# Kernel tuning notes

Hardware: AMD Instinct MI355X
Metric: run time of the kernel (lower is better)

Reference implementation:

```python
import jax, jax.numpy as jnp
import numpy as np

# ---- constants mirroring the torch module ----
OSAMP = 8            # temporal oversampling factor
MAX_ITER = 10        # forward solver iterations (LBFGS replaced by fixed GD)
NEG_SHIFT = 2 * OSAMP
OTP = 5              # baseline frames subtracted from ctc/aif
C_SHARP = 500.0      # sharpness constant C=500 in fermi_ir_func
LR = 0.1             # fixed step size for the deterministic forward solve


def interp_linear_1d(x, size):
    # interp_linear_1D: linear upsampling along last (time) axis
    return jax.image.resize(x, x.shape[:-1] + (size,), method='linear')


def fermi_ir(eta, t_os):
    # eta: [B,3,H,W] = (amplitude A, decay rate k, delay t0); t_os: [Tos]
    tsh = t_os - t_os[NEG_SHIFT]                    # negative time shift
    A = eta[:, 0][..., None]                        # [B,H,W,1]
    k = eta[:, 1][..., None]
    t0 = eta[:, 2][..., None]
    step = jax.nn.sigmoid(C_SHARP * tsh)            # sharp causal onset (C=500)
    return A * jax.nn.sigmoid(k * (t0 - tsh)) * step  # [B,H,W,Tos]


def convolve(aif, ir):
    # linear convolution along time via FFT; output aligned with neg_shift offset
    Tos = ir.shape[-1]
    n = 2 * Tos
    Fa = jnp.fft.rfft(aif, n=n, axis=-1)            # [B,1,1,n/2+1]
    Fi = jnp.fft.rfft(ir, n=n, axis=-1)             # [B,H,W,n/2+1]
    full = jnp.fft.irfft(Fa * Fi, n=n, axis=-1)
    return jax.lax.dynamic_slice_in_dim(full, NEG_SHIFT, Tos, axis=-1)


def make_objective(ctc, aif, time, eta_prior, lambda_reg):
    # preprocessing from FermiDataConsLBFGS.forward
    aif = aif - aif[..., :OTP].mean(-1, keepdims=True)
    ctc = ctc - ctc[..., :OTP].mean(-1, keepdims=True)
    Tos = OSAMP * ctc.shape[-1]
    aif_os = interp_linear_1d(aif, Tos)
    ctc_os = interp_linear_1d(ctc, Tos)
    t_os = interp_linear_1d(time, Tos)
    ctc_dc = ctc_os[..., ::OSAMP]                   # [B,H,W,T]
    C_nn = (eta_prior ** 2).sum(axis=(0, 2, 3), keepdims=True)  # [1,3,1,1]
    C_dc = (ctc_dc ** 2).sum()
    sp_lam = jax.nn.softplus(lambda_reg).squeeze()

    def F_obj(eta):  # FermiDConsObj.__call__ (OD disabled: indx_dc = all frames)
        ir = fermi_ir(eta, t_os)
        ctc_est = convolve(aif_os, ir)[..., ::OSAMP] / OSAMP
        dc = ((ctc_dc - ctc_est) ** 2 / C_dc).sum()
        reg = sp_lam * (((eta - eta_prior) ** 2) / C_nn).sum()
        pos = (jax.nn.relu(-eta) ** 2).sum()
        return dc + reg + pos
    return F_obj


def setup_inputs():
    key = jax.random.key(0)
    k1, k2, k3, k4 = jax.random.split(key, 4)
    B, H, W, T = 1, 128, 128, 64
    ctc = jax.random.normal(k1, (B, H, W, T), jnp.float32) * 0.1
    aif = jax.random.uniform(k2, (B, 1, 1, T), jnp.float32)
    time = jnp.arange(T, dtype=jnp.float32)
    seg = jnp.ones((B, H, W), jnp.int32)
    eta_nn = jax.random.uniform(k3, (B, 3, H, W), jnp.float32)
    lambda_reg = jax.random.normal(k4, (1,), jnp.float32)
    return {"ctc": ctc, "aif": aif, "time": time, "seg": seg,
            "eta_nn": eta_nn, "lambda_reg": lambda_reg}


def reference(ctc, aif, time, seg, eta_nn, lambda_reg):
    # seg only affects the (disabled) outlier-detection path
    F_obj = make_objective(ctc, aif, time, eta_nn, lambda_reg)
    gradF = jax.grad(F_obj)

    def step(eta, _):
        return eta - LR * gradF(eta), None

    eta_pi, _ = jax.lax.scan(step, eta_nn, None, length=MAX_ITER)
    return eta_pi
```

## Files before the change

### kernel.cpp

```cpp
#include <hip/hip_runtime.h>
#include <math.h>

#define T_IN 64
#define NPIX 16384
#define MAX_ITER 10
#define NSLOT 43

typedef _Float16 half8_t __attribute__((ext_vector_type(8)));
typedef __fp16   fp16x2  __attribute__((ext_vector_type(2)));
typedef float    f32x4   __attribute__((ext_vector_type(4)));
typedef int      i32x4   __attribute__((ext_vector_type(4)));

union H8 { half8_t v; fp16x2 h2[4]; i32x4 i4; };

__device__ __forceinline__ float rcp_fast(float x) { return __builtin_amdgcn_rcpf(x); }

__device__ __forceinline__ float exp2_fast(float x) {
#if __has_builtin(__builtin_amdgcn_exp2f)
    return __builtin_amdgcn_exp2f(x);
#else
    return exp2f(x);
#endif
}

__constant__ constexpr int NTMIN[16] = {0,0,0,0,0,1,1,1,1,2,2,2,2,3,3,3};
__constant__ constexpr int TOFS[16]  = {0,4,8,12,16,20,23,26,29,32,34,36,38,40,41,42};
__constant__ constexpr int POS[16]   = {0,0,4,4,8,8,12,11,15,14,18,16,20,18,22,19};
#define NBREG 23

template<int KT>
__device__ __forceinline__ void buildTile(float T0, float c, float cT0, float ch,
        float r, float r2, float r3, int q,
        const float (&d10s)[8], const float (&tse)[8],
        H8& F0h, H8& F1h, H8& F2h) {
    constexpr int J = KT >> 1;
    float  x[8];
    fp16x2 d1h[4];
    float  d10 = T0 - d10s[J];
    const fp16x2 c1 = {(__fp16)0.25f, (__fp16)0.25f};
    const fp16x2 c2 = {(__fp16)0.50f, (__fp16)0.50f};
    const fp16x2 c3 = {(__fp16)0.75f, (__fp16)0.75f};
    bool arith = true;
    if constexpr (KT == 0 || KT == 15) {
        bool flat = (KT == 0) ? (q == 0) : (q == 3);
        if (flat) {
            arith = false;
            #pragma unroll
            for (int j = 0; j < 8; ++j)
                x[j] = exp2_fast(fmaf(-c, tse[j], cT0));
            #pragma unroll
            for (int jj = 0; jj < 4; ++jj)
                d1h[jj] = __builtin_amdgcn_cvt_pkrtz(T0 - tse[2*jj],
                                                     T0 - tse[2*jj+1]);
        }
    }
    if (arith) {
        float a0 = fmaf(-c, d10s[J], cT0);
        x[0] = exp2_fast(a0);
        x[4] = exp2_fast(a0 - ch);
        x[1] = x[0]*r; x[2] = x[0]*r2; x[3] = x[0]*r3;
        x[5] = x[4]*r; x[6] = x[4]*r2; x[7] = x[4]*r3;
        fp16x2 D0 = __builtin_amdgcn_cvt_pkrtz(d10, d10 - 0.125f);
        d1h[0] = D0;
        d1h[1] = D0 - c1;
        d1h[2] = D0 - c2;
        d1h[3] = D0 - c3;
    }
    #pragma unroll
    for (int jj = 0; jj < 4; ++jj) {
        float s1a = rcp_fast(1.0f + x[2*jj]);
        float s1b = rcp_fast(1.0f + x[2*jj+1]);
        fp16x2 sh = __builtin_amdgcn_cvt_pkrtz(s1a, s1b);
        fp16x2 eh = sh - sh*sh;
        F0h.h2[jj] = sh;
        F1h.h2[jj] = eh * d1h[jj];
        F2h.h2[jj] = eh;
    }
}

template<int KT, int NT, int BI>
struct MfmaNT {
    static __device__ __forceinline__ void run(const i32x4 (&Breg)[NBREG],
            const H8 (&F0p)[4], const H8 (&F1p)[4], const H8 (&F2p)[4],
            f32x4 (&acc)[3][4]) {
        constexpr int idx = POS[KT] + NT - NTMIN[KT];
        H8 bh; bh.i4 = Breg[idx];
        if constexpr (KT < 2) {
            const f32x4 Z = (f32x4){0.f, 0.f, 0.f, 0.f};
            acc[0][NT] = __builtin_amdgcn_mfma_f32_16x16x32_f16(F0p[BI].v, bh.v, Z, 0, 0, 0);
            acc[1][NT] = __builtin_amdgcn_mfma_f32_16x16x32_f16(F1p[BI].v, bh.v, Z, 0, 0, 0);
            acc[2][NT] = __builtin_amdgcn_mfma_f32_16x16x32_f16(F2p[BI].v, bh.v, Z, 0, 0, 0);
        } else {
            acc[0][NT] = __builtin_amdgcn_mfma_f32_16x16x32_f16(F0p[BI].v, bh.v, acc[0][NT], 0, 0, 0);
            acc[1][NT] = __builtin_amdgcn_mfma_f32_16x16x32_f16(F1p[BI].v, bh.v, acc[1][NT], 0, 0, 0);
            acc[2][NT] = __builtin_amdgcn_mfma_f32_16x16x32_f16(F2p[BI].v, bh.v, acc[2][NT], 0, 0, 0);
        }
        if constexpr (NT + 1 < 4)
            MfmaNT<KT, NT+1, BI>::run(Breg, F0p, F1p, F2p, acc);
    }
};

template<int H, int S>
struct PipeB {
    static __device__ __forceinline__ void run(float T0, float c, float cT0, float ch,
            float r, float r2, float r3, int q,
            const float (&d10s)[8], const float (&tse)[8],
            const i32x4 (&Breg)[NBREG],
            H8 (&F0p)[4], H8 (&F1p)[4], H8 (&F2p)[4],
            f32x4 (&acc)[3][4]) {
        if constexpr (2*S+2 < 8)
            buildTile<H + 2*(2*S+2)>(T0, c, cT0, ch, r, r2, r3, q, d10s, tse,
                F0p[(2*S+2)&3], F1p[(2*S+2)&3], F2p[(2*S+2)&3]);
        if constexpr (2*S+3 < 8)
            buildTile<H + 2*(2*S+3)>(T0, c, cT0, ch, r, r2, r3, q, d10s, tse,
                F0p[(2*S+3)&3], F1p[(2*S+3)&3], F2p[(2*S+3)&3]);
        MfmaNT<H + 4*S,     NTMIN[H + 4*S],     (2*S)&3  >::run(Breg, F0p, F1p, F2p, acc);
        MfmaNT<H + 4*S + 2, NTMIN[H + 4*S + 2], (2*S+1)&3>::run(Breg, F0p, F1p, F2p, acc);
        if constexpr (S + 1 < 4)
            PipeB<H, S+1>::run(T0, c, cT0, ch, r, r2, r3, q, d10s, tse,
                               Breg, F0p, F1p, F2p, acc);
    }
};

template<int H>
__device__ __forceinline__ void pipeAcc(float T0, float c, float cT0, float ch,
        float r, float r2, float r3, int q,
        const float (&d10s)[8], const float (&tse)[8],
        const i32x4 (&Breg)[NBREG], f32x4 (&acc)[3][4]) {
    H8 F0p[4], F1p[4], F2p[4];
    buildTile<H>  (T0, c, cT0, ch, r, r2, r3, q, d10s, tse, F0p[0], F1p[0], F2p[0]);
    buildTile<H+2>(T0, c, cT0, ch, r, r2, r3, q, d10s, tse, F0p[1], F1p[1], F2p[1]);
    PipeB<H, 0>::run(T0, c, cT0, ch, r, r2, r3, q, d10s, tse, Breg, F0p, F1p, F2p, acc);
}

template<int KT, int NT>
struct LoadNT {
    static __device__ __forceinline__ void run(const i32x4* __restrict__ Bgl,
                                               i32x4 (&Breg)[NBREG]) {
        Breg[POS[KT] + NT - NTMIN[KT]] = Bgl[(TOFS[KT] + NT - NTMIN[KT]) * 64];
        if constexpr (NT + 1 < 4) LoadNT<KT, NT+1>::run(Bgl, Breg);
    }
};
template<int KT>
struct LoadB {
    static __device__ __forceinline__ void run(const i32x4* __restrict__ Bgl,
                                               i32x4 (&Breg)[NBREG]) {
        LoadNT<KT, NTMIN[KT]>::run(Bgl, Breg);
        if constexpr (KT + 2 < 16) LoadB<KT+2>::run(Bgl, Breg);
    }
};

template<int H>
__device__ __forceinline__ void sendHalf(const f32x4 (&acc)[3][4],
        float2* __restrict__ xch, int pair, int lane) {
    constexpr int SB = 2 - 2*H;
    float2* xw = xch + ((pair*2 + H)*12)*64 + lane;
    #pragma unroll
    for (int i = 0; i < 3; ++i)
        #pragma unroll
        for (int nt = 0; nt < 4; ++nt)
            xw[(i*4+nt)*64] = make_float2(acc[i][nt][SB], acc[i][nt][SB+1]);
}

template<int H>
__device__ __forceinline__ void finishDots(f32x4 (&acc)[3][4],
        const float2* __restrict__ xch, float (&Gtab)[2][16][4],
        int pair, int lane, int q, int n,
        const float (&dch)[4][2], float A) {
    constexpr int KB = 2*H;
    const float2* xr = xch + ((pair*2 + (1-H))*12)*64 + lane;
    #pragma unroll
    for (int i = 0; i < 3; ++i)
        #pragma unroll
        for (int nt = 0; nt < 4; ++nt) {
            float2 v = xr[(i*4+nt)*64];
            acc[i][nt][KB]   += v.x;
            acc[i][nt][KB+1] += v.y;
        }
    float Ap0 = __shfl(A, q*4 + KB);
    float Ap1 = __shfl(A, q*4 + KB + 1);
    float SA0=0.f,SK0=0.f,ST0=0.f, SA1=0.f,SK1=0.f,ST1=0.f;
    #pragma unroll
    for (int nt = 0; nt < 4; ++nt) {
        float Y0 = acc[0][nt][KB], Y1 = acc[1][nt][KB], Y2 = acc[2][nt][KB];
        float rr = fmaf(Ap0, Y0, -dch[nt][0]);
        SA0 = fmaf(rr, Y0, SA0); SK0 = fmaf(rr, Y1, SK0); ST0 = fmaf(rr, Y2, ST0);
        float y0 = acc[0][nt][KB+1], y1 = acc[1][nt][KB+1], y2 = acc[2][nt][KB+1];
        float r2 = fmaf(Ap1, y0, -dch[nt][1]);
        SA1 = fmaf(r2, y0, SA1); SK1 = fmaf(r2, y1, SK1); ST1 = fmaf(r2, y2, ST1);
    }
    #pragma unroll
    for (int m = 1; m < 16; m <<= 1) {
        SA0 += __shfl_xor(SA0, m); SK0 += __shfl_xor(SK0, m); ST0 += __shfl_xor(ST0, m);
        SA1 += __shfl_xor(SA1, m); SK1 += __shfl_xor(SK1, m); ST1 += __shfl_xor(ST1, m);
    }
    if (n == 0) {
        float* g = Gtab[pair][q*4 + KB];
        g[0] = SA0; g[1] = SK0; g[2] = ST0;
    }
    if (n == 1) {
        float* g = Gtab[pair][q*4 + KB + 1];
        g[0] = SA1; g[1] = SK1; g[2] = ST1;
    }
}

__global__ __launch_bounds__(256, 1) void k_prep(
        const float* __restrict__ ctc,  const float* __restrict__ aif,
        const float* __restrict__ timev,const float* __restrict__ eta,
        float* __restrict__ tshg, i32x4* __restrict__ Bg,
        f32x4* __restrict__ partials) {
    __shared__ float tshs[512];
    __shared__ float aifos[512];
    __shared__ float a_s[64], t_s[64];
    __shared__ f32x4 red[4];

    const int tid  = threadIdx.x;
    const int lane = tid & 63;
    const int wid  = tid >> 6;
    const int q = lane >> 4, n = lane & 15;
    const int pixbase = blockIdx.x * 64 + wid * 16;
    const int mypix   = pixbase + n;

    if (tid < 64) { a_s[tid] = aif[tid]; t_s[tid] = timev[tid]; }
    float A  = eta[mypix];
    float K  = eta[NPIX + mypix];
    float T0 = eta[2*NPIX + mypix];
    __syncthreads();
    {
        float m5a = 0.2f * (a_s[0]+a_s[1]+a_s[2]+a_s[3]+a_s[4]);
        float t16;
        {
            float xx = 1.5625f; int i0 = (int)xx; float f = xx - (float)i0;
            t16 = t_s[i0]*(1.0f-f) + t_s[i0+1]*f;
        }
        #pragma unroll
        for (int rep = 0; rep < 2; ++rep) {
            int i = tid + 256*rep;
            float x = ((float)i - 3.5f) * 0.125f;
            float ao, to;
            if (x <= 0.0f)       { ao = a_s[0]  - m5a; to = t_s[0];  }
            else if (x >= 63.0f) { ao = a_s[63] - m5a; to = t_s[63]; }
            else {
                int i0 = (int)x; float f = x - (float)i0;
                ao = (a_s[i0]-m5a)*(1.0f-f) + (a_s[i0+1]-m5a)*f;
                to = t_s[i0]*(1.0f-f) + t_s[i0+1]*f;
            }
            aifos[i] = ao;
            tshs[i]  = to - t16;
            if (blockIdx.x == 0) tshg[i] = to - t16;
        }
    }
    __syncthreads();

    if (blockIdx.x < NSLOT && tid < 64) {
        int slot = blockIdx.x, l = tid;
        int kt, nt;
        if (slot < 20)      { kt = slot >> 2; nt = slot & 3; }
        else if (slot < 32) { int s = slot - 20; int d3 = s / 3; kt = 5 + d3; nt = 1 + (s - 3*d3); }
        else if (slot < 40) { int s = slot - 32; kt = 9 + (s >> 1); nt = 2 + (s & 1); }
        else                { kt = 13 + (slot - 40); nt = 3; }
        int kbase = 32*kt + 8*(l >> 4);
        int m = 16 + 8 * (16*nt + (l & 15));
        H8 bh;
        #pragma unroll
        for (int jj = 0; jj < 4; ++jj) {
            float v[2];
            #pragma unroll
            for (int h = 0; h < 2; ++h) {
                int k  = kbase + 2*jj + h;
                int ai = m - k;
                float s2 = 1.0f / (1.0f + __expf(-500.0f * tshs[k]));
                v[h] = (ai >= 0 && ai < 512) ? s2 * aifos[ai] * 0.125f : 0.0f;
            }
            bh.h2[jj] = (fp16x2){(__fp16)v[0], (__fp16)v[1]};
        }
        Bg[slot*64 + l] = bh.i4;
    }

    float vs = 0.f;
    #pragma unroll
    for (int reg = 0; reg < 4; ++reg) {
        const float* cp = ctc + (pixbase + q*4 + reg) * T_IN;
        float m5 = 0.2f * (cp[0]+cp[1]+cp[2]+cp[3]+cp[4]);
        #pragma unroll
        for (int nt = 0; nt < 4; ++nt) {
            int d = nt*16 + n;
            float cc = cp[d] - m5;
            float cm = cp[(d > 0) ? d-1 : 0] - m5;
            float dc = (d == 0) ? cc : (0.4375f*cm + 0.5625f*cc);
            vs += dc * dc;
        }
    }
    {
        f32x4 pv = (f32x4){vs, 0.25f*A*A, 0.25f*K*K, 0.25f*T0*T0};
        #pragma unroll
        for (int m = 1; m < 64; m <<= 1) {
            pv.x += __shfl_xor(pv.x, m); pv.y += __shfl_xor(pv.y, m);
            pv.z += __shfl_xor(pv.z, m); pv.w += __shfl_xor(pv.w, m);
        }
        if (lane == 0) red[wid] = pv;
    }
    __syncthreads();
    if (tid == 0)
        partials[blockIdx.x] = red[0] + red[1] + red[2] + red[3];
}

__global__ __launch_bounds__(256, 2) void k_iter(
        const float* __restrict__ ctc,  const float* __restrict__ lam,
        const float* __restrict__ eta,  const float* __restrict__ tshg,
        const i32x4* __restrict__ Bg,   const f32x4* __restrict__ partials,
        float* __restrict__ out) {
    __shared__ float2 xch[2*2*12*64];
    __shared__ float Gtab[2][16][4];

    const int tid  = threadIdx.x;
    const int lane = tid & 63;
    const int wid  = tid >> 6;
    const int hh   = wid & 1;
    const int pair = wid >> 1;
    const int q = lane >> 4, n = lane & 15;
    const int pixbase = blockIdx.x * 32 + pair * 16;
    const int mypix   = pixbase + n;

    const i32x4* Bgl = Bg + lane;
    i32x4 Breg[NBREG];
    if (hh == 0) LoadB<0>::run(Bgl, Breg);
    else         LoadB<1>::run(Bgl, Breg);

    float A  = eta[mypix];
    float K  = eta[NPIX + mypix];
    float T0 = eta[2*NPIX + mypix];
    const float pA = A, pK = K, pT = T0;

    float dch[4][2];
    #pragma unroll
    for (int j = 0; j < 2; ++j) {
        const float* cp = ctc + (pixbase + q*4 + 2*hh + j) * T_IN;
        float m5 = 0.2f * (cp[0]+cp[1]+cp[2]+cp[3]+cp[4]);
        #pragma unroll
        for (int nt = 0; nt < 4; ++nt) {
            int d = nt*16 + n;
            float cc = cp[d] - m5;
            float cm = cp[(d > 0) ? d-1 : 0] - m5;
            dch[nt][j] = (d == 0) ? cc : (0.4375f*cm + 0.5625f*cc);
        }
    }

    float d10s[8];
    #pragma unroll
    for (int j = 0; j < 8; ++j) d10s[j] = tshg[32*(2*j + hh) + 8*q];
    float tse[8];
    {
        const float* tb = hh ? (tshg + 480) : tshg;
        #pragma unroll
        for (int j = 0; j < 8; ++j) tse[j] = tb[8*q + j];
    }

    f32x4 tot = partials[lane] + partials[64+lane] + partials[128+lane]
              + partials[192+lane];
    #pragma unroll
    for (int m = 1; m < 64; m <<= 1) {
        tot.x += __shfl_xor(tot.x, m); tot.y += __shfl_xor(tot.y, m);
        tot.z += __shfl_xor(tot.z, m); tot.w += __shfl_xor(tot.w, m);
    }
    float spl;
    {
        float xl = lam[0];
        spl = (xl > 0.0f) ? (xl + log1pf(__expf(-xl))) : log1pf(__expf(xl));
    }
    const float cdc2 = 2.0f / tot.x;
    const float rgA  = 2.0f * spl / tot.y;
    const float rgK  = 2.0f * spl / tot.z;
    const float rgT  = 2.0f * spl / tot.w;

    #pragma unroll 1
    for (int it = 0; it < MAX_ITER; ++it) {
        float c   = -1.44269504f * K;
        float cT0 = c * T0;
        float ch  = 0.5f * c;
        float r   = exp2_fast(0.18033688f * K);
        float r2  = r * r;
        float r3  = r2 * r;

        f32x4 acc[3][4];
        if (hh == 0) {
            pipeAcc<0>(T0, c, cT0, ch, r, r2, r3, q, d10s, tse, Breg, acc);
            sendHalf<0>(acc, xch, pair, lane);
        } else {
            pipeAcc<1>(T0, c, cT0, ch, r, r2, r3, q, d10s, tse, Breg, acc);
            sendHalf<1>(acc, xch, pair, lane);
        }
        __syncthreads();
        if (hh == 0) finishDots<0>(acc, xch, Gtab, pair, lane, q, n, dch, A);
        else         finishDots<1>(acc, xch, Gtab, pair, lane, q, n, dch, A);
        __syncthreads();

        const float GA = Gtab[pair][n][0];
        const float GK = Gtab[pair][n][1];
        const float GT = Gtab[pair][n][2];
        float gA = fmaf(rgA, A  - pA, cdc2 * GA)         + 2.0f * fminf(A,  0.f);
        float gK = fmaf(rgK, K  - pK, cdc2 * A * GK)     + 2.0f * fminf(K,  0.f);
        float gT = fmaf(rgT, T0 - pT, cdc2 * A * K * GT) + 2.0f * fminf(T0, 0.f);
        A  -= 0.1f * gA;
        K  -= 0.1f * gK;
        T0 -= 0.1f * gT;
    }

    if (hh == 0 && lane < 16) {
        out[mypix]          = A;
        out[NPIX + mypix]   = K;
        out[2*NPIX + mypix] = T0;
    }
}

extern "C" void kernel_launch(void* const* d_in, const int* in_sizes, int n_in,
                              void* d_out, int out_size, void* d_ws, size_t ws_size,
                              hipStream_t stream) {
    const float* ctc   = (const float*)d_in[0];
    const float* aif   = (const float*)d_in[1];
    const float* timev = (const float*)d_in[2];
    const float* eta   = (const float*)d_in[4];
    const float* lam   = (const float*)d_in[5];
    float* out = (float*)d_out;
    f32x4* partials = (f32x4*)d_ws;
    float* tshg     = (float*)((char*)d_ws + 4096);
    i32x4* Bg       = (i32x4*)((char*)d_ws + 8192);

    k_prep<<<NPIX / 64, 256, 0, stream>>>(ctc, aif, timev, eta,
                                          tshg, Bg, partials);
    k_iter<<<NPIX / 32, 256, 0, stream>>>(ctc, lam, eta, tshg, Bg,
                                          partials, out);
}
```

Before: 103.3 us.

## Split output N-tiles across four waves per 16-pixel group, stream B from global

Each block now handles 16 pixels with four waves. The waves split both the K halves and the output column tiles, so each wave accumulates only two N-tiles instead of four. The B-matrix fragments are no longer preloaded into 23 registers; they are loaded from global memory one step ahead inside the MFMA pipeline. Partial gradients from the two N-tile waves are summed through shared memory. Launch bounds rise to 4 blocks per CU and the grid doubles, aiming for higher occupancy and lower register pressure at the cost of redundant sigmoid tile builds and repeated global/L2 loads of B every iteration.

```diff
diff --git a/kernel.cpp b/kernel.cpp
--- a/kernel.cpp
+++ b/kernel.cpp
@@ -25,8 +25,6 @@
 
 __constant__ constexpr int NTMIN[16] = {0,0,0,0,0,1,1,1,1,2,2,2,2,3,3,3};
 __constant__ constexpr int TOFS[16]  = {0,4,8,12,16,20,23,26,29,32,34,36,38,40,41,42};
-__constant__ constexpr int POS[16]   = {0,0,4,4,8,8,12,11,15,14,18,16,20,18,22,19};
-#define NBREG 23
 
 template<int KT>
 __device__ __forceinline__ void buildTile(float T0, float c, float cT0, float ch,
@@ -78,129 +76,128 @@
     }
 }
 
-template<int KT, int NT, int BI>
-struct MfmaNT {
-    static __device__ __forceinline__ void run(const i32x4 (&Breg)[NBREG],
-            const H8 (&F0p)[4], const H8 (&F1p)[4], const H8 (&F2p)[4],
-            f32x4 (&acc)[3][4]) {
-        constexpr int idx = POS[KT] + NT - NTMIN[KT];
-        H8 bh; bh.i4 = Breg[idx];
-        if constexpr (KT < 2) {
-            const f32x4 Z = (f32x4){0.f, 0.f, 0.f, 0.f};
-            acc[0][NT] = __builtin_amdgcn_mfma_f32_16x16x32_f16(F0p[BI].v, bh.v, Z, 0, 0, 0);
-            acc[1][NT] = __builtin_amdgcn_mfma_f32_16x16x32_f16(F1p[BI].v, bh.v, Z, 0, 0, 0);
-            acc[2][NT] = __builtin_amdgcn_mfma_f32_16x16x32_f16(F2p[BI].v, bh.v, Z, 0, 0, 0);
-        } else {
-            acc[0][NT] = __builtin_amdgcn_mfma_f32_16x16x32_f16(F0p[BI].v, bh.v, acc[0][NT], 0, 0, 0);
-            acc[1][NT] = __builtin_amdgcn_mfma_f32_16x16x32_f16(F1p[BI].v, bh.v, acc[1][NT], 0, 0, 0);
-            acc[2][NT] = __builtin_amdgcn_mfma_f32_16x16x32_f16(F2p[BI].v, bh.v, acc[2][NT], 0, 0, 0);
-        }
-        if constexpr (NT + 1 < 4)
-            MfmaNT<KT, NT+1, BI>::run(Breg, F0p, F1p, F2p, acc);
+template<int KT, int M, int BI>
+struct MfmaT {
+    static __device__ __forceinline__ void run(const i32x4 b0, const i32x4 b1,
+            const H8 (&F0p)[2], const H8 (&F1p)[2], const H8 (&F2p)[2],
+            f32x4 (&acc)[3][2]) {
+        const f32x4 Z = (f32x4){0.f, 0.f, 0.f, 0.f};
+        if constexpr (M >= NTMIN[KT]) {
+            H8 bh; bh.i4 = b0;
+            if constexpr (KT < 2) {
+                acc[0][0] = __builtin_amdgcn_mfma_f32_16x16x32_f16(F0p[BI].v, bh.v, Z, 0, 0, 0);
+                acc[1][0] = __builtin_amdgcn_mfma_f32_16x16x32_f16(F1p[BI].v, bh.v, Z, 0, 0, 0);
+                acc[2][0] = __builtin_amdgcn_mfma_f32_16x16x32_f16(F2p[BI].v, bh.v, Z, 0, 0, 0);
+            } else {
+                acc[0][0] = __builtin_amdgcn_mfma_f32_16x16x32_f16(F0p[BI].v, bh.v, acc[0][0], 0, 0, 0);
+                acc[1][0] = __builtin_amdgcn_mfma_f32_16x16x32_f16(F1p[BI].v, bh.v, acc[1][0], 0, 0, 0);
+                acc[2][0] = __builtin_amdgcn_mfma_f32_16x16x32_f16(F2p[BI].v, bh.v, acc[2][0], 0, 0, 0);
+            }
+        }
+        if constexpr (M + 2 >= NTMIN[KT]) {
+            H8 bh; bh.i4 = b1;
+            if constexpr (KT < 2) {
+                acc[0][1] = __builtin_amdgcn_mfma_f32_16x16x32_f16(F0p[BI].v, bh.v, Z, 0, 0, 0);
+                acc[1][1] = __builtin_amdgcn_mfma_f32_16x16x32_f16(F1p[BI].v, bh.v, Z, 0, 0, 0);
+                acc[2][1] = __builtin_amdgcn_mfma_f32_16x16x32_f16(F2p[BI].v, bh.v, Z, 0, 0, 0);
+            } else {
+                acc[0][1] = __builtin_amdgcn_mfma_f32_16x16x32_f16(F0p[BI].v, bh.v, acc[0][1], 0, 0, 0);
+                acc[1][1] = __builtin_amdgcn_mfma_f32_16x16x32_f16(F1p[BI].v, bh.v, acc[1][1], 0, 0, 0);
+                acc[2][1] = __builtin_amdgcn_mfma_f32_16x16x32_f16(F2p[BI].v, bh.v, acc[2][1], 0, 0, 0);
+            }
+        }
     }
 };
 
-template<int H, int S>
-struct PipeB {
+template<int H, int M, int I>
+struct PipeHM {
     static __device__ __forceinline__ void run(float T0, float c, float cT0, float ch,
             float r, float r2, float r3, int q,
             const float (&d10s)[8], const float (&tse)[8],
-            const i32x4 (&Breg)[NBREG],
-            H8 (&F0p)[4], H8 (&F1p)[4], H8 (&F2p)[4],
-            f32x4 (&acc)[3][4]) {
-        if constexpr (2*S+2 < 8)
-            buildTile<H + 2*(2*S+2)>(T0, c, cT0, ch, r, r2, r3, q, d10s, tse,
-                F0p[(2*S+2)&3], F1p[(2*S+2)&3], F2p[(2*S+2)&3]);
-        if constexpr (2*S+3 < 8)
-            buildTile<H + 2*(2*S+3)>(T0, c, cT0, ch, r, r2, r3, q, d10s, tse,
-                F0p[(2*S+3)&3], F1p[(2*S+3)&3], F2p[(2*S+3)&3]);
-        MfmaNT<H + 4*S,     NTMIN[H + 4*S],     (2*S)&3  >::run(Breg, F0p, F1p, F2p, acc);
-        MfmaNT<H + 4*S + 2, NTMIN[H + 4*S + 2], (2*S+1)&3>::run(Breg, F0p, F1p, F2p, acc);
-        if constexpr (S + 1 < 4)
-            PipeB<H, S+1>::run(T0, c, cT0, ch, r, r2, r3, q, d10s, tse,
-                               Breg, F0p, F1p, F2p, acc);
+            const i32x4* __restrict__ Bgl,
+            const i32x4 b0, const i32x4 b1,
+            H8 (&F0p)[2], H8 (&F1p)[2], H8 (&F2p)[2],
+            f32x4 (&acc)[3][2]) {
+        constexpr int KT = H + 2*I;
+        i32x4 nb0 = (i32x4){0,0,0,0}, nb1 = (i32x4){0,0,0,0};
+        if constexpr (I + 1 < 8) {
+            constexpr int KN = KT + 2;
+            if constexpr (M >= NTMIN[KN])
+                nb0 = Bgl[(TOFS[KN] + M - NTMIN[KN]) * 64];
+            if constexpr (M + 2 >= NTMIN[KN])
+                nb1 = Bgl[(TOFS[KN] + (M+2) - NTMIN[KN]) * 64];
+            buildTile<KN>(T0, c, cT0, ch, r, r2, r3, q, d10s, tse,
+                          F0p[(I+1)&1], F1p[(I+1)&1], F2p[(I+1)&1]);
+        }
+        MfmaT<KT, M, I&1>::run(b0, b1, F0p, F1p, F2p, acc);
+        if constexpr (I + 1 < 8)
+            PipeHM<H, M, I+1>::run(T0, c, cT0, ch, r, r2, r3, q, d10s, tse,
+                                   Bgl, nb0, nb1, F0p, F1p, F2p, acc);
     }
 };
 
-template<int H>
-__device__ __forceinline__ void pipeAcc(float T0, float c, float cT0, float ch,
+template<int H, int M>
+__device__ __forceinline__ void pipeAcc2(float T0, float c, float cT0, float ch,
         float r, float r2, float r3, int q,
         const float (&d10s)[8], const float (&tse)[8],
-        const i32x4 (&Breg)[NBREG], f32x4 (&acc)[3][4]) {
-    H8 F0p[4], F1p[4], F2p[4];
-    buildTile<H>  (T0, c, cT0, ch, r, r2, r3, q, d10s, tse, F0p[0], F1p[0], F2p[0]);
-    buildTile<H+2>(T0, c, cT0, ch, r, r2, r3, q, d10s, tse, F0p[1], F1p[1], F2p[1]);
-    PipeB<H, 0>::run(T0, c, cT0, ch, r, r2, r3, q, d10s, tse, Breg, F0p, F1p, F2p, acc);
-}
-
-template<int KT, int NT>
-struct LoadNT {
-    static __device__ __forceinline__ void run(const i32x4* __restrict__ Bgl,
-                                               i32x4 (&Breg)[NBREG]) {
-        Breg[POS[KT] + NT - NTMIN[KT]] = Bgl[(TOFS[KT] + NT - NTMIN[KT]) * 64];
-        if constexpr (NT + 1 < 4) LoadNT<KT, NT+1>::run(Bgl, Breg);
-    }
-};
-template<int KT>
-struct LoadB {
-    static __device__ __forceinline__ void run(const i32x4* __restrict__ Bgl,
-                                               i32x4 (&Breg)[NBREG]) {
-        LoadNT<KT, NTMIN[KT]>::run(Bgl, Breg);
-        if constexpr (KT + 2 < 16) LoadB<KT+2>::run(Bgl, Breg);
-    }
-};
+        const i32x4* __restrict__ Bgl, f32x4 (&acc)[3][2]) {
+    H8 F0p[2], F1p[2], F2p[2];
+    i32x4 b0 = Bgl[(TOFS[H] + M) * 64];
+    i32x4 b1 = Bgl[(TOFS[H] + M + 2) * 64];
+    buildTile<H>(T0, c, cT0, ch, r, r2, r3, q, d10s, tse, F0p[0], F1p[0], F2p[0]);
+    PipeHM<H, M, 0>::run(T0, c, cT0, ch, r, r2, r3, q, d10s, tse, Bgl, b0, b1,
+                         F0p, F1p, F2p, acc);
+}
 
 template<int H>
-__device__ __forceinline__ void sendHalf(const f32x4 (&acc)[3][4],
-        float2* __restrict__ xch, int pair, int lane) {
+__device__ __forceinline__ void sendHalf2(const f32x4 (&acc)[3][2],
+        float2* __restrict__ xch, int m, int lane) {
     constexpr int SB = 2 - 2*H;
-    float2* xw = xch + ((pair*2 + H)*12)*64 + lane;
+    float2* xw = xch + ((m*2 + H)*6)*64 + lane;
     #pragma unroll
     for (int i = 0; i < 3; ++i)
         #pragma unroll
-        for (int nt = 0; nt < 4; ++nt)
-            xw[(i*4+nt)*64] = make_float2(acc[i][nt][SB], acc[i][nt][SB+1]);
+        for (int a = 0; a < 2; ++a)
+            xw[(i*2+a)*64] = make_float2(acc[i][a][SB], acc[i][a][SB+1]);
 }
 
 template<int H>
-__device__ __forceinline__ void finishDots(f32x4 (&acc)[3][4],
-        const float2* __restrict__ xch, float (&Gtab)[2][16][4],
-        int pair, int lane, int q, int n,
-        const float (&dch)[4][2], float A) {
+__device__ __forceinline__ void finishDots2(f32x4 (&acc)[3][2],
+        const float2* __restrict__ xch, float (&xs2)[2][4][4][3],
+        int m, int lane, int q, int n,
+        const float (&dch)[2][2], float A) {
     constexpr int KB = 2*H;
-    const float2* xr = xch + ((pair*2 + (1-H))*12)*64 + lane;
+    const float2* xr = xch + ((m*2 + (1-H))*6)*64 + lane;
     #pragma unroll
     for (int i = 0; i < 3; ++i)
         #pragma unroll
-        for (int nt = 0; nt < 4; ++nt) {
-            float2 v = xr[(i*4+nt)*64];
-            acc[i][nt][KB]   += v.x;
-            acc[i][nt][KB+1] += v.y;
+        for (int a = 0; a < 2; ++a) {
+            float2 v = xr[(i*2+a)*64];
+            acc[i][a][KB]   += v.x;
+            acc[i][a][KB+1] += v.y;
         }
     float Ap0 = __shfl(A, q*4 + KB);
     float Ap1 = __shfl(A, q*4 + KB + 1);
     float SA0=0.f,SK0=0.f,ST0=0.f, SA1=0.f,SK1=0.f,ST1=0.f;
     #pragma unroll
-    for (int nt = 0; nt < 4; ++nt) {
-        float Y0 = acc[0][nt][KB], Y1 = acc[1][nt][KB], Y2 = acc[2][nt][KB];
-        float rr = fmaf(Ap0, Y0, -dch[nt][0]);
+    for (int a = 0; a < 2; ++a) {
+        float Y0 = acc[0][a][KB], Y1 = acc[1][a][KB], Y2 = acc[2][a][KB];
+        float rr = fmaf(Ap0, Y0, -dch[a][0]);
         SA0 = fmaf(rr, Y0, SA0); SK0 = fmaf(rr, Y1, SK0); ST0 = fmaf(rr, Y2, ST0);
-        float y0 = acc[0][nt][KB+1], y1 = acc[1][nt][KB+1], y2 = acc[2][nt][KB+1];
-        float r2 = fmaf(Ap1, y0, -dch[nt][1]);
+        float y0 = acc[0][a][KB+1], y1 = acc[1][a][KB+1], y2 = acc[2][a][KB+1];
+        float r2 = fmaf(Ap1, y0, -dch[a][1]);
         SA1 = fmaf(r2, y0, SA1); SK1 = fmaf(r2, y1, SK1); ST1 = fmaf(r2, y2, ST1);
     }
     #pragma unroll
-    for (int m = 1; m < 16; m <<= 1) {
-        SA0 += __shfl_xor(SA0, m); SK0 += __shfl_xor(SK0, m); ST0 += __shfl_xor(ST0, m);
-        SA1 += __shfl_xor(SA1, m); SK1 += __shfl_xor(SK1, m); ST1 += __shfl_xor(ST1, m);
+    for (int mm = 1; mm < 16; mm <<= 1) {
+        SA0 += __shfl_xor(SA0, mm); SK0 += __shfl_xor(SK0, mm); ST0 += __shfl_xor(ST0, mm);
+        SA1 += __shfl_xor(SA1, mm); SK1 += __shfl_xor(SK1, mm); ST1 += __shfl_xor(ST1, mm);
     }
     if (n == 0) {
-        float* g = Gtab[pair][q*4 + KB];
-        g[0] = SA0; g[1] = SK0; g[2] = ST0;
+        xs2[m][q][KB][0] = SA0; xs2[m][q][KB][1] = SK0; xs2[m][q][KB][2] = ST0;
     }
     if (n == 1) {
-        float* g = Gtab[pair][q*4 + KB + 1];
-        g[0] = SA1; g[1] = SK1; g[2] = ST1;
+        xs2[m][q][KB+1][0] = SA1; xs2[m][q][KB+1][1] = SK1; xs2[m][q][KB+1][2] = ST1;
     }
 }
 
@@ -305,53 +302,50 @@
         partials[blockIdx.x] = red[0] + red[1] + red[2] + red[3];
 }
 
-__global__ __launch_bounds__(256, 2) void k_iter(
+__global__ __launch_bounds__(256, 4) void k_iter(
         const float* __restrict__ ctc,  const float* __restrict__ lam,
         const float* __restrict__ eta,  const float* __restrict__ tshg,
         const i32x4* __restrict__ Bg,   const f32x4* __restrict__ partials,
         float* __restrict__ out) {
-    __shared__ float2 xch[2*2*12*64];
-    __shared__ float Gtab[2][16][4];
+    __shared__ float2 xch[2*2*6*64];
+    __shared__ float  xs2[2][4][4][3];
 
     const int tid  = threadIdx.x;
     const int lane = tid & 63;
     const int wid  = tid >> 6;
-    const int hh   = wid & 1;
-    const int pair = wid >> 1;
+    const int h    = wid & 1;
+    const int m    = wid >> 1;
     const int q = lane >> 4, n = lane & 15;
-    const int pixbase = blockIdx.x * 32 + pair * 16;
+    const int pixbase = blockIdx.x * 16;
     const int mypix   = pixbase + n;
 
     const i32x4* Bgl = Bg + lane;
-    i32x4 Breg[NBREG];
-    if (hh == 0) LoadB<0>::run(Bgl, Breg);
-    else         LoadB<1>::run(Bgl, Breg);
 
     float A  = eta[mypix];
     float K  = eta[NPIX + mypix];
     float T0 = eta[2*NPIX + mypix];
     const float pA = A, pK = K, pT = T0;
 
-    float dch[4][2];
+    float dch[2][2];
     #pragma unroll
     for (int j = 0; j < 2; ++j) {
-        const float* cp = ctc + (pixbase + q*4 + 2*hh + j) * T_IN;
+        const float* cp = ctc + (pixbase + q*4 + 2*h + j) * T_IN;
         float m5 = 0.2f * (cp[0]+cp[1]+cp[2]+cp[3]+cp[4]);
         #pragma unroll
-        for (int nt = 0; nt < 4; ++nt) {
-            int d = nt*16 + n;
+        for (int a = 0; a < 2; ++a) {
+            int d = (m + 2*a)*16 + n;
             float cc = cp[d] - m5;
             float cm = cp[(d > 0) ? d-1 : 0] - m5;
-            dch[nt][j] = (d == 0) ? cc : (0.4375f*cm + 0.5625f*cc);
+            dch[a][j] = (d == 0) ? cc : (0.4375f*cm + 0.5625f*cc);
         }
     }
 
     float d10s[8];
     #pragma unroll
-    for (int j = 0; j < 8; ++j) d10s[j] = tshg[32*(2*j + hh) + 8*q];
+    for (int j = 0; j < 8; ++j) d10s[j] = tshg[32*(2*j + h) + 8*q];
     float tse[8];
     {
-        const float* tb = hh ? (tshg + 480) : tshg;
+        const float* tb = h ? (tshg + 480) : tshg;
         #pragma unroll
         for (int j = 0; j < 8; ++j) tse[j] = tb[8*q + j];
     }
@@ -359,9 +353,9 @@
     f32x4 tot = partials[lane] + partials[64+lane] + partials[128+lane]
               + partials[192+lane];
     #pragma unroll
-    for (int m = 1; m < 64; m <<= 1) {
-        tot.x += __shfl_xor(tot.x, m); tot.y += __shfl_xor(tot.y, m);
-        tot.z += __shfl_xor(tot.z, m); tot.w += __shfl_xor(tot.w, m);
+    for (int mm = 1; mm < 64; mm <<= 1) {
+        tot.x += __shfl_xor(tot.x, mm); tot.y += __shfl_xor(tot.y, mm);
+        tot.z += __shfl_xor(tot.z, mm); tot.w += __shfl_xor(tot.w, mm);
     }
     float spl;
     {
@@ -382,22 +376,24 @@
         float r2  = r * r;
         float r3  = r2 * r;
 
-        f32x4 acc[3][4];
-        if (hh == 0) {
-            pipeAcc<0>(T0, c, cT0, ch, r, r2, r3, q, d10s, tse, Breg, acc);
-            sendHalf<0>(acc, xch, pair, lane);
-        } else {
-            pipeAcc<1>(T0, c, cT0, ch, r, r2, r3, q, d10s, tse, Breg, acc);
-            sendHalf<1>(acc, xch, pair, lane);
-        }
+        f32x4 acc[3][2];
+        if      (wid == 0) { pipeAcc2<0,0>(T0,c,cT0,ch,r,r2,r3,q,d10s,tse,Bgl,acc);
+                             sendHalf2<0>(acc, xch, 0, lane); }
+        else if (wid == 1) { pipeAcc2<1,0>(T0,c,cT0,ch,r,r2,r3,q,d10s,tse,Bgl,acc);
+                             sendHalf2<1>(acc, xch, 0, lane); }
+        else if (wid == 2) { pipeAcc2<0,1>(T0,c,cT0,ch,r,r2,r3,q,d10s,tse,Bgl,acc);
+                             sendHalf2<0>(acc, xch, 1, lane); }
+        else               { pipeAcc2<1,1>(T0,c,cT0,ch,r,r2,r3,q,d10s,tse,Bgl,acc);
+                             sendHalf2<1>(acc, xch, 1, lane); }
         __syncthreads();
-        if (hh == 0) finishDots<0>(acc, xch, Gtab, pair, lane, q, n, dch, A);
-        else         finishDots<1>(acc, xch, Gtab, pair, lane, q, n, dch, A);
+        if (h == 0) finishDots2<0>(acc, xch, xs2, m, lane, q, n, dch, A);
+        else        finishDots2<1>(acc, xch, xs2, m, lane, q, n, dch, A);
         __syncthreads();
 
-        const float GA = Gtab[pair][n][0];
-        const float GK = Gtab[pair][n][1];
-        const float GT = Gtab[pair][n][2];
+        const int qp = n >> 2, cpx = n & 3;
+        const float GA = xs2[0][qp][cpx][0] + xs2[1][qp][cpx][0];
+        const float GK = xs2[0][qp][cpx][1] + xs2[1][qp][cpx][1];
+        const float GT = xs2[0][qp][cpx][2] + xs2[1][qp][cpx][2];
         float gA = fmaf(rgA, A  - pA, cdc2 * GA)         + 2.0f * fminf(A,  0.f);
         float gK = fmaf(rgK, K  - pK, cdc2 * A * GK)     + 2.0f * fminf(K,  0.f);
         float gT = fmaf(rgT, T0 - pT, cdc2 * A * K * GT) + 2.0f * fminf(T0, 0.f);
@@ -406,7 +402,7 @@
         T0 -= 0.1f * gT;
     }
 
-    if (hh == 0 && lane < 16) {
+    if (wid == 0 && lane < 16) {
         out[mypix]          = A;
         out[NPIX + mypix]   = K;
         out[2*NPIX + mypix] = T0;
@@ -428,6 +424,6 @@
 
     k_prep<<<NPIX / 64, 256, 0, stream>>>(ctc, aif, timev, eta,
                                           tshg, Bg, partials);
-    k_iter<<<NPIX / 32, 256, 0, stream>>>(ctc, lam, eta, tshg, Bg,
+    k_iter<<<NPIX / 16, 256, 0, stream>>>(ctc, lam, eta, tshg, Bg,
                                           partials, out);
 }
```

Result: slower. 146.4 us (+41.7%).
